# Kernel tuning notes

Measured on AMD Instinct MI355X. Metric: run time of the kernel, lower is better.

## Reference

```python
import jax, jax.numpy as jnp
import numpy as np
import math

EPS = 1e-5  # torch nn.LayerNorm default
MODEL_DIM = 1024


def _layernorm(x, g, b):
    mu = jnp.mean(x, axis=-1, keepdims=True)
    var = jnp.mean(jnp.square(x - mu), axis=-1, keepdims=True)
    return (x - mu) * jax.lax.rsqrt(var + EPS) * g + b


def _block(x, g, b, w, bias):
    # LayerNorm -> Linear -> exact (erf) GELU, matching torch nn.GELU default
    h = _layernorm(x, g, b)
    h = h @ w.T + bias
    return jax.nn.gelu(h, approximate=False)


def setup_inputs() -> dict:
    key = jax.random.key(0)
    ks = jax.random.split(key, 4)
    N, F = 262144, 6
    dims = [F, 128, 512, 1024]
    inp = {"x": jax.random.normal(ks[0], (N, F), dtype=jnp.float32)}
    for i in range(3):
        fan_in, fan_out = dims[i], dims[i + 1]
        bound = 1.0 / math.sqrt(fan_in)
        inp[f"ln{i}_g"] = jnp.ones((fan_in,), dtype=jnp.float32)
        inp[f"ln{i}_b"] = jnp.zeros((fan_in,), dtype=jnp.float32)
        inp[f"w{i}"] = jax.random.uniform(ks[i + 1], (fan_out, fan_in), dtype=jnp.float32, minval=-bound, maxval=bound)
        inp[f"b{i}"] = jnp.zeros((fan_out,), dtype=jnp.float32)
    return inp


def reference(x, ln0_g, ln0_b, w0, b0, ln1_g, ln1_b, w1, b1, ln2_g, ln2_b, w2, b2):
    h = _block(x, ln0_g, ln0_b, w0, b0)
    h = _block(h, ln1_g, ln1_b, w1, b1)
    h = _block(h, ln2_g, ln2_b, w2, b2)
    return h * jnp.float32(math.sqrt(MODEL_DIM))
```

## Files before the change

### kernel.cpp

```cpp
#include <hip/hip_runtime.h>

typedef __attribute__((ext_vector_type(8))) __bf16 bf16x8;
typedef __attribute__((ext_vector_type(4))) float f32x4;
typedef __attribute__((ext_vector_type(8))) unsigned short ushort8;
typedef __attribute__((ext_vector_type(4))) float floatx4;

__device__ __forceinline__ unsigned short f2bf(float f) {
    return __builtin_bit_cast(unsigned short, (__bf16)f);
}
__device__ __forceinline__ float bf2f(unsigned short s) {
    return (float)__builtin_bit_cast(__bf16, s);
}
__device__ __forceinline__ float gelu_f(float v) {
    return 0.5f * v * (1.0f + erff(v * 0.70710678118654752440f));
}

__device__ __forceinline__ char* h1_at(unsigned short* h1, int row, int col) {
    return (char*)h1 + row * 256 + ((col * 2) ^ ((row & 7) << 4));
}
__device__ __forceinline__ char* h2_at(unsigned short* h2, int row, int col) {
    return (char*)h2 + row * 1024 + ((col * 2) ^ ((row & 7) << 4));
}

template<bool BF>
__device__ __forceinline__ bf16x8 load_w8(const void* wp, int off) {
    if constexpr (BF) {
        return *(const bf16x8*)((const unsigned short*)wp + off);
    } else {
        const float* p = (const float*)wp + off;
        floatx4 lo = *(const floatx4*)p;
        floatx4 hi = *(const floatx4*)(p + 4);
        union { unsigned short u[8]; bf16x8 v; } pk;
        #pragma unroll
        for (int e = 0; e < 4; ++e) { pk.u[e] = f2bf(lo[e]); pk.u[4 + e] = f2bf(hi[e]); }
        return pk.v;
    }
}

__global__ void prep_kernel(const float* __restrict__ w1, const float* __restrict__ w2,
                            unsigned short* __restrict__ w1b, unsigned short* __restrict__ w2b) {
    int i = blockIdx.x * 256 + threadIdx.x;
    if (i < 512 * 128) w1b[i] = f2bf(w1[i]);
    int j = i - 512 * 128;
    if (j >= 0 && j < 1024 * 512) w2b[j] = f2bf(w2[j]);
}

template<bool BF>
__global__ __launch_bounds__(256, 2) void fused_mlp(
    const float* __restrict__ x,
    const float* __restrict__ ln0g, const float* __restrict__ ln0b,
    const float* __restrict__ w0,   const float* __restrict__ b0,
    const float* __restrict__ ln1g, const float* __restrict__ ln1b,
    const void*  __restrict__ w1p,  const float* __restrict__ b1,
    const float* __restrict__ ln2g, const float* __restrict__ ln2b,
    const void*  __restrict__ w2p,  const float* __restrict__ b2,
    float* __restrict__ out)
{
    __shared__ alignas(16) unsigned short h1n[64 * 128];
    __shared__ alignas(16) unsigned short h2s[64 * 512];

    const int tid  = threadIdx.x;
    const int lane = tid & 63;
    const int wv   = tid >> 6;
    const long rowbase = (long)blockIdx.x * 64;

    if (tid < 64) {
        const int r = tid;
        const long grow = rowbase + r;
        float xv[6], xn[6];
        #pragma unroll
        for (int f = 0; f < 6; ++f) xv[f] = x[grow * 6 + f];
        float mu = 0.f;
        #pragma unroll
        for (int f = 0; f < 6; ++f) mu += xv[f];
        mu *= (1.0f / 6.0f);
        float var = 0.f;
        #pragma unroll
        for (int f = 0; f < 6; ++f) { float d = xv[f] - mu; var += d * d; }
        var *= (1.0f / 6.0f);
        const float rstd = rsqrtf(var + 1e-5f);
        #pragma unroll
        for (int f = 0; f < 6; ++f) xn[f] = (xv[f] - mu) * rstd * ln0g[f] + ln0b[f];

        float s1 = 0.f, s2 = 0.f;
        #pragma unroll 1
        for (int n = 0; n < 128; ++n) {
            float a = b0[n];
            #pragma unroll
            for (int f = 0; f < 6; ++f) a += xn[f] * w0[n * 6 + f];
            a = gelu_f(a);
            s1 += a; s2 += a * a;
        }
        const float mu1   = s1 * (1.0f / 128.0f);
        const float var1  = s2 * (1.0f / 128.0f) - mu1 * mu1;
        const float rstd1 = rsqrtf(var1 + 1e-5f);

        #pragma unroll 1
        for (int g = 0; g < 16; ++g) {
            union { unsigned short u[8]; ushort8 v; } pk;
            #pragma unroll
            for (int e = 0; e < 8; ++e) {
                const int n = g * 8 + e;
                float a = b0[n];
                #pragma unroll
                for (int f = 0; f < 6; ++f) a += xn[f] * w0[n * 6 + f];
                a = gelu_f(a);
                pk.u[e] = f2bf((a - mu1) * rstd1 * ln1g[n] + ln1b[n]);
            }
            *(ushort8*)h1_at(h1n, r, g * 8) = pk.v;
        }
    }
    __syncthreads();

    {
        const int lr = lane & 15;
        const int lk = (lane >> 4) * 8;
        const int mr = (lane >> 4) * 4;
        #pragma unroll 1
        for (int c = 0; c < 2; ++c) {
            const int n0 = wv * 128 + c * 64;
            f32x4 acc[4][4] = {};
            #pragma unroll
            for (int ks = 0; ks < 4; ++ks) {
                const int k0 = ks * 32 + lk;
                bf16x8 af[4], bfv[4];
                #pragma unroll
                for (int i = 0; i < 4; ++i)
                    af[i] = *(const bf16x8*)h1_at(h1n, i * 16 + lr, k0);
                #pragma unroll
                for (int j = 0; j < 4; ++j)
                    bfv[j] = load_w8<BF>(w1p, (n0 + j * 16 + lr) * 128 + k0);
                #pragma unroll
                for (int i = 0; i < 4; ++i)
                    #pragma unroll
                    for (int j = 0; j < 4; ++j)
                        acc[i][j] = __builtin_amdgcn_mfma_f32_16x16x32_bf16(af[i], bfv[j], acc[i][j], 0, 0, 0);
            }
            #pragma unroll
            for (int j = 0; j < 4; ++j) {
                const int n = n0 + j * 16 + lr;
                const float bias = b1[n];
                #pragma unroll
                for (int i = 0; i < 4; ++i)
                    #pragma unroll
                    for (int rr = 0; rr < 4; ++rr) {
                        const int m = i * 16 + mr + rr;
                        *(unsigned short*)h2_at(h2s, m, n) = f2bf(gelu_f(acc[i][j][rr] + bias));
                    }
            }
        }
    }
    __syncthreads();

    if (tid < 64) {
        const int r = tid;
        float s1 = 0.f, s2 = 0.f;
        #pragma unroll 1
        for (int g = 0; g < 64; ++g) {
            ushort8 v = *(const ushort8*)h2_at(h2s, r, g * 8);
            #pragma unroll
            for (int e = 0; e < 8; ++e) { const float f = bf2f(v[e]); s1 += f; s2 += f * f; }
        }
        const float mu   = s1 * (1.0f / 512.0f);
        const float var  = s2 * (1.0f / 512.0f) - mu * mu;
        const float rstd = rsqrtf(var + 1e-5f);
        #pragma unroll 1
        for (int g = 0; g < 64; ++g) {
            char* p = h2_at(h2s, r, g * 8);
            ushort8 v = *(const ushort8*)p;
            union { unsigned short u[8]; ushort8 vv; } pk;
            #pragma unroll
            for (int e = 0; e < 8; ++e) {
                const int n = g * 8 + e;
                pk.u[e] = f2bf((bf2f(v[e]) - mu) * rstd * ln2g[n] + ln2b[n]);
            }
            *(ushort8*)p = pk.vv;
        }
    }
    __syncthreads();

    {
        const int lr = lane & 15;
        const int lk = (lane >> 4) * 8;
        const int mr = (lane >> 4) * 4;
        #pragma unroll 1
        for (int c = 0; c < 4; ++c) {
            const int n0 = wv * 256 + c * 64;
            f32x4 acc[4][4] = {};
            #pragma unroll 1
            for (int ks = 0; ks < 16; ++ks) {
                const int k0 = ks * 32 + lk;
                bf16x8 af[4], bfv[4];
                #pragma unroll
                for (int i = 0; i < 4; ++i)
                    af[i] = *(const bf16x8*)h2_at(h2s, i * 16 + lr, k0);
                #pragma unroll
                for (int j = 0; j < 4; ++j)
                    bfv[j] = load_w8<BF>(w2p, (n0 + j * 16 + lr) * 512 + k0);
                #pragma unroll
                for (int i = 0; i < 4; ++i)
                    #pragma unroll
                    for (int j = 0; j < 4; ++j)
                        acc[i][j] = __builtin_amdgcn_mfma_f32_16x16x32_bf16(af[i], bfv[j], acc[i][j], 0, 0, 0);
            }
            #pragma unroll
            for (int j = 0; j < 4; ++j) {
                const int n = n0 + j * 16 + lr;
                const float bias = b2[n];
                #pragma unroll
                for (int i = 0; i < 4; ++i)
                    #pragma unroll
                    for (int rr = 0; rr < 4; ++rr) {
                        const int m = i * 16 + mr + rr;
                        out[(rowbase + m) * 1024 + n] = gelu_f(acc[i][j][rr] + bias) * 32.0f;
                    }
            }
        }
    }
}

extern "C" void kernel_launch(void* const* d_in, const int* in_sizes, int n_in,
                              void* d_out, int out_size, void* d_ws, size_t ws_size,
                              hipStream_t stream)
{
    const float* x    = (const float*)d_in[0];
    const float* ln0g = (const float*)d_in[1];
    const float* ln0b = (const float*)d_in[2];
    const float* w0   = (const float*)d_in[3];
    const float* b0   = (const float*)d_in[4];
    const float* ln1g = (const float*)d_in[5];
    const float* ln1b = (const float*)d_in[6];
    const float* w1   = (const float*)d_in[7];
    const float* b1   = (const float*)d_in[8];
    const float* ln2g = (const float*)d_in[9];
    const float* ln2b = (const float*)d_in[10];
    const float* w2   = (const float*)d_in[11];
    const float* b2   = (const float*)d_in[12];
    float* out = (float*)d_out;

    const int rows = in_sizes[0] / 6;
    const int grid = rows / 64;
    const size_t need = (size_t)(512 * 128 + 1024 * 512) * sizeof(unsigned short);

    if (ws_size >= need) {
        unsigned short* w1b = (unsigned short*)d_ws;
        unsigned short* w2b = w1b + 512 * 128;
        prep_kernel<<<dim3((512 * 128 + 1024 * 512 + 255) / 256), dim3(256), 0, stream>>>(w1, w2, w1b, w2b);
        fused_mlp<true><<<dim3(grid), dim3(256), 0, stream>>>(
            x, ln0g, ln0b, w0, b0, ln1g, ln1b, (const void*)w1b, b1,
            ln2g, ln2b, (const void*)w2b, b2, out);
    } else {
        fused_mlp<false><<<dim3(grid), dim3(256), 0, stream>>>(
            x, ln0g, ln0b, w0, b0, ln1g, ln1b, (const void*)w1, b1,
            ln2g, ln2b, (const void*)w2, b2, out);
    }
}
```

Measured before the change: 1.232 ms.

## Parallelize layernorm phases across all threads and double-buffer MFMA fragment loads

The layer-0 and layernorm-2 phases now use all 256 threads, four per row, with partial sums reduced through LDS scratch, where before only 64 threads worked. Layer-0 GELU outputs are kept in registers instead of being recomputed in a second pass. Both GEMM loops now use ping-pong fragment registers so that global and LDS loads for the next k-step overlap the current MFMAs. Output stores are nontemporal. The cost is more register pressure from h0[32] and the doubled fragments, which could hurt occupancy under the launch bound of 2 blocks per CU.

```diff
diff --git a/kernel.cpp b/kernel.cpp
--- a/kernel.cpp
+++ b/kernel.cpp
@@ -15,11 +15,8 @@
     return 0.5f * v * (1.0f + erff(v * 0.70710678118654752440f));
 }
 
-__device__ __forceinline__ char* h1_at(unsigned short* h1, int row, int col) {
-    return (char*)h1 + row * 256 + ((col * 2) ^ ((row & 7) << 4));
-}
-__device__ __forceinline__ char* h2_at(unsigned short* h2, int row, int col) {
-    return (char*)h2 + row * 1024 + ((col * 2) ^ ((row & 7) << 4));
+__device__ __forceinline__ char* lds_at(unsigned short* base, int rowBytes, int row, int col) {
+    return (char*)base + row * rowBytes + ((col * 2) ^ ((row & 7) << 4));
 }
 
 template<bool BF>
@@ -35,6 +32,27 @@
         for (int e = 0; e < 4; ++e) { pk.u[e] = f2bf(lo[e]); pk.u[4 + e] = f2bf(hi[e]); }
         return pk.v;
     }
+}
+
+__device__ __forceinline__ void load_afrag(bf16x8 (&dst)[4], unsigned short* lds,
+                                           int rowBytes, int lr, int k0) {
+    #pragma unroll
+    for (int i = 0; i < 4; ++i)
+        dst[i] = *(const bf16x8*)lds_at(lds, rowBytes, i * 16 + lr, k0);
+}
+template<bool BF>
+__device__ __forceinline__ void load_bfrag(bf16x8 (&dst)[4], const void* wp,
+                                           int ldk, int ncol, int k0) {
+    #pragma unroll
+    for (int j = 0; j < 4; ++j)
+        dst[j] = load_w8<BF>(wp, (ncol + j * 16) * ldk + k0);
+}
+__device__ __forceinline__ void mm16(f32x4 (&acc)[4][4], const bf16x8 (&a)[4], const bf16x8 (&b)[4]) {
+    #pragma unroll
+    for (int i = 0; i < 4; ++i)
+        #pragma unroll
+        for (int j = 0; j < 4; ++j)
+            acc[i][j] = __builtin_amdgcn_mfma_f32_16x16x32_bf16(a[i], b[j], acc[i][j], 0, 0, 0);
 }
 
 __global__ void prep_kernel(const float* __restrict__ w1, const float* __restrict__ w2,
@@ -64,8 +82,9 @@
     const int wv   = tid >> 6;
     const long rowbase = (long)blockIdx.x * 64;
 
-    if (tid < 64) {
-        const int r = tid;
+    {
+        const int r = tid >> 2;
+        const int q = tid & 3;
         const long grow = rowbase + r;
         float xv[6], xn[6];
         #pragma unroll
@@ -82,32 +101,35 @@
         #pragma unroll
         for (int f = 0; f < 6; ++f) xn[f] = (xv[f] - mu) * rstd * ln0g[f] + ln0b[f];
 
+        float h0[32];
         float s1 = 0.f, s2 = 0.f;
-        #pragma unroll 1
-        for (int n = 0; n < 128; ++n) {
+        #pragma unroll
+        for (int o = 0; o < 32; ++o) {
+            const int n = q * 32 + o;
             float a = b0[n];
             #pragma unroll
             for (int f = 0; f < 6; ++f) a += xn[f] * w0[n * 6 + f];
             a = gelu_f(a);
-            s1 += a; s2 += a * a;
-        }
+            h0[o] = a; s1 += a; s2 += a * a;
+        }
+        float* scr = (float*)h2s;
+        scr[tid] = s1; scr[256 + tid] = s2;
+        __syncthreads();
+        const int b4 = tid & ~3;
+        s1 = scr[b4] + scr[b4 + 1] + scr[b4 + 2] + scr[b4 + 3];
+        s2 = scr[256 + b4] + scr[256 + b4 + 1] + scr[256 + b4 + 2] + scr[256 + b4 + 3];
         const float mu1   = s1 * (1.0f / 128.0f);
         const float var1  = s2 * (1.0f / 128.0f) - mu1 * mu1;
         const float rstd1 = rsqrtf(var1 + 1e-5f);
-
-        #pragma unroll 1
-        for (int g = 0; g < 16; ++g) {
+        #pragma unroll
+        for (int o8 = 0; o8 < 4; ++o8) {
             union { unsigned short u[8]; ushort8 v; } pk;
             #pragma unroll
             for (int e = 0; e < 8; ++e) {
-                const int n = g * 8 + e;
-                float a = b0[n];
-                #pragma unroll
-                for (int f = 0; f < 6; ++f) a += xn[f] * w0[n * 6 + f];
-                a = gelu_f(a);
-                pk.u[e] = f2bf((a - mu1) * rstd1 * ln1g[n] + ln1b[n]);
-            }
-            *(ushort8*)h1_at(h1n, r, g * 8) = pk.v;
+                const int n = q * 32 + o8 * 8 + e;
+                pk.u[e] = f2bf((h0[o8 * 8 + e] - mu1) * rstd1 * ln1g[n] + ln1b[n]);
+            }
+            *(ushort8*)lds_at(h1n, 256, r, q * 32 + o8 * 8) = pk.v;
         }
     }
     __syncthreads();
@@ -120,22 +142,19 @@
         for (int c = 0; c < 2; ++c) {
             const int n0 = wv * 128 + c * 64;
             f32x4 acc[4][4] = {};
-            #pragma unroll
-            for (int ks = 0; ks < 4; ++ks) {
-                const int k0 = ks * 32 + lk;
-                bf16x8 af[4], bfv[4];
-                #pragma unroll
-                for (int i = 0; i < 4; ++i)
-                    af[i] = *(const bf16x8*)h1_at(h1n, i * 16 + lr, k0);
-                #pragma unroll
-                for (int j = 0; j < 4; ++j)
-                    bfv[j] = load_w8<BF>(w1p, (n0 + j * 16 + lr) * 128 + k0);
-                #pragma unroll
-                for (int i = 0; i < 4; ++i)
-                    #pragma unroll
-                    for (int j = 0; j < 4; ++j)
-                        acc[i][j] = __builtin_amdgcn_mfma_f32_16x16x32_bf16(af[i], bfv[j], acc[i][j], 0, 0, 0);
-            }
+            bf16x8 aP[4], bP[4], aQ[4], bQ[4];
+            load_afrag(aP, h1n, 256, lr, lk);
+            load_bfrag<BF>(bP, w1p, 128, n0 + lr, lk);
+            load_afrag(aQ, h1n, 256, lr, 32 + lk);
+            load_bfrag<BF>(bQ, w1p, 128, n0 + lr, 32 + lk);
+            mm16(acc, aP, bP);
+            load_afrag(aP, h1n, 256, lr, 64 + lk);
+            load_bfrag<BF>(bP, w1p, 128, n0 + lr, 64 + lk);
+            mm16(acc, aQ, bQ);
+            load_afrag(aQ, h1n, 256, lr, 96 + lk);
+            load_bfrag<BF>(bQ, w1p, 128, n0 + lr, 96 + lk);
+            mm16(acc, aP, bP);
+            mm16(acc, aQ, bQ);
             #pragma unroll
             for (int j = 0; j < 4; ++j) {
                 const int n = n0 + j * 16 + lr;
@@ -145,35 +164,41 @@
                     #pragma unroll
                     for (int rr = 0; rr < 4; ++rr) {
                         const int m = i * 16 + mr + rr;
-                        *(unsigned short*)h2_at(h2s, m, n) = f2bf(gelu_f(acc[i][j][rr] + bias));
+                        *(unsigned short*)lds_at(h2s, 1024, m, n) = f2bf(gelu_f(acc[i][j][rr] + bias));
                     }
             }
         }
     }
     __syncthreads();
 
-    if (tid < 64) {
-        const int r = tid;
+    {
+        const int r = tid >> 2;
+        const int q = tid & 3;
         float s1 = 0.f, s2 = 0.f;
-        #pragma unroll 1
-        for (int g = 0; g < 64; ++g) {
-            ushort8 v = *(const ushort8*)h2_at(h2s, r, g * 8);
+        #pragma unroll
+        for (int g = 0; g < 16; ++g) {
+            ushort8 v = *(const ushort8*)lds_at(h2s, 1024, r, q * 128 + g * 8);
             #pragma unroll
             for (int e = 0; e < 8; ++e) { const float f = bf2f(v[e]); s1 += f; s2 += f * f; }
         }
+        float* scr = (float*)h1n;
+        scr[tid] = s1; scr[256 + tid] = s2;
+        __syncthreads();
+        const int b4 = tid & ~3;
+        s1 = scr[b4] + scr[b4 + 1] + scr[b4 + 2] + scr[b4 + 3];
+        s2 = scr[256 + b4] + scr[256 + b4 + 1] + scr[256 + b4 + 2] + scr[256 + b4 + 3];
         const float mu   = s1 * (1.0f / 512.0f);
         const float var  = s2 * (1.0f / 512.0f) - mu * mu;
         const float rstd = rsqrtf(var + 1e-5f);
-        #pragma unroll 1
-        for (int g = 0; g < 64; ++g) {
-            char* p = h2_at(h2s, r, g * 8);
+        #pragma unroll
+        for (int g = 0; g < 16; ++g) {
+            const int col0 = q * 128 + g * 8;
+            char* p = lds_at(h2s, 1024, r, col0);
             ushort8 v = *(const ushort8*)p;
             union { unsigned short u[8]; ushort8 vv; } pk;
             #pragma unroll
-            for (int e = 0; e < 8; ++e) {
-                const int n = g * 8 + e;
-                pk.u[e] = f2bf((bf2f(v[e]) - mu) * rstd * ln2g[n] + ln2b[n]);
-            }
+            for (int e = 0; e < 8; ++e)
+                pk.u[e] = f2bf((bf2f(v[e]) - mu) * rstd * ln2g[col0 + e] + ln2b[col0 + e]);
             *(ushort8*)p = pk.vv;
         }
     }
@@ -187,21 +212,20 @@
         for (int c = 0; c < 4; ++c) {
             const int n0 = wv * 256 + c * 64;
             f32x4 acc[4][4] = {};
-            #pragma unroll 1
-            for (int ks = 0; ks < 16; ++ks) {
+            bf16x8 aP[4], bP[4], aQ[4], bQ[4];
+            load_afrag(aP, h2s, 1024, lr, lk);
+            load_bfrag<BF>(bP, w2p, 512, n0 + lr, lk);
+            #pragma unroll
+            for (int ks = 0; ks < 16; ks += 2) {
                 const int k0 = ks * 32 + lk;
-                bf16x8 af[4], bfv[4];
-                #pragma unroll
-                for (int i = 0; i < 4; ++i)
-                    af[i] = *(const bf16x8*)h2_at(h2s, i * 16 + lr, k0);
-                #pragma unroll
-                for (int j = 0; j < 4; ++j)
-                    bfv[j] = load_w8<BF>(w2p, (n0 + j * 16 + lr) * 512 + k0);
-                #pragma unroll
-                for (int i = 0; i < 4; ++i)
-                    #pragma unroll
-                    for (int j = 0; j < 4; ++j)
-                        acc[i][j] = __builtin_amdgcn_mfma_f32_16x16x32_bf16(af[i], bfv[j], acc[i][j], 0, 0, 0);
+                load_afrag(aQ, h2s, 1024, lr, k0 + 32);
+                load_bfrag<BF>(bQ, w2p, 512, n0 + lr, k0 + 32);
+                mm16(acc, aP, bP);
+                if (ks + 2 < 16) {
+                    load_afrag(aP, h2s, 1024, lr, k0 + 64);
+                    load_bfrag<BF>(bP, w2p, 512, n0 + lr, k0 + 64);
+                }
+                mm16(acc, aQ, bQ);
             }
             #pragma unroll
             for (int j = 0; j < 4; ++j) {
@@ -212,7 +236,8 @@
                     #pragma unroll
                     for (int rr = 0; rr < 4; ++rr) {
                         const int m = i * 16 + mr + rr;
-                        out[(rowbase + m) * 1024 + n] = gelu_f(acc[i][j][rr] + bias) * 32.0f;
+                        const float v = gelu_f(acc[i][j][rr] + bias) * 32.0f;
+                        __builtin_nontemporal_store(v, &out[(rowbase + m) * 1024 + n]);
                     }
             }
         }
```

Result: slower. 1.390 ms (+12.8%).
